# Kernel optimization log

Hardware: AMD Instinct MI355X
Metric: run time of the kernel (lower is better)

The kernel has to match this reference:

```python
import jax, jax.numpy as jnp
import numpy as np

B, C, H, W = 32, 64, 96, 96
RED = 8


def setup_inputs() -> dict:
    key = jax.random.key(0)
    k0, k1, k2 = jax.random.split(key, 3)
    x = jax.random.normal(k0, (B, C, H, W), dtype=jnp.float32)
    # 1x1 conv weights (squeezed to linear): conv1 C->C//RED, conv2 C//RED->C
    w1 = jax.random.normal(k1, (C // RED, C), dtype=jnp.float32) * (1.0 / np.sqrt(C))
    b1 = jnp.zeros((C // RED,), dtype=jnp.float32)
    w2 = jax.random.normal(k2, (C, C // RED), dtype=jnp.float32) * (1.0 / np.sqrt(C // RED))
    b2 = jnp.zeros((C,), dtype=jnp.float32)
    return {"x": x, "w1": w1, "b1": b1, "w2": w2, "b2": b2}


def reference(x, w1, b1, w2, b2):
    Bx, Cx, Hx, Wx = x.shape
    M = Hx * Wx
    # --- covariance pooling: x @ I_hat @ x^T == centered outer product / M ---
    xr = x.reshape(Bx, Cx, M)
    xc = xr - xr.mean(axis=-1, keepdims=True)
    cov = jnp.einsum('bcm,bdm->bcd', xc, xc) / M  # (B, C, C)
    # --- Newton-Schulz matrix sqrt, iteration = 5 ---
    I3 = 3.0 * jnp.eye(Cx, dtype=x.dtype)  # broadcast over batch
    normA = jnp.trace(cov, axis1=1, axis2=2)  # (1/3 * cov * 3I).sum == trace
    A = cov / normA[:, None, None]
    ZY = 0.5 * (I3 - A)
    Y = A @ ZY
    Z = ZY
    for _ in range(3):  # range(1, iteration-1) with iteration=5
        ZY = (0.5 * (I3 - Z)) @ Y
        Y = Y @ ZY
        Z = ZY @ Z
    ZY = 0.5 * (Y @ (I3 - Z @ Y))
    cov_sqrt = ZY * jnp.sqrt(normA)[:, None, None]  # (B, C, C)
    # --- channel gating ---
    s = cov_sqrt.mean(axis=1)  # mean over dim=1 -> (B, C)
    h = jax.nn.relu(s @ w1.T + b1)
    gate = jax.nn.sigmoid(h @ w2.T + b2)  # (B, C)
    return x * gate[:, :, None, None]
```

## Files before the change

kernel.cpp:

```cpp
#include <hip/hip_runtime.h>
#include <math.h>


#define BB 32
#define CC 64
#define MM 9216

typedef __attribute__((ext_vector_type(8))) short bf16x8;
typedef __attribute__((ext_vector_type(4))) float f32x4;

__device__ __forceinline__ short f2bf(float f) {
  unsigned u = __builtin_bit_cast(unsigned, f);
  return (short)(unsigned short)((u + 0x8000u) >> 16);
}
__device__ __forceinline__ float bf2f(short h) {
  unsigned u = ((unsigned)(unsigned short)h) << 16;
  return __builtin_bit_cast(float, u);
}

#define NCHUNK 8
#define CHUNK_M (MM / NCHUNK)
#define WAVE_M (CHUNK_M / 4)
#define NSTEP (WAVE_M / 32)

__global__ __launch_bounds__(256) void gram_k(const float* __restrict__ x,
                                              float* __restrict__ covws,
                                              float* __restrict__ sumws) {
  int b = blockIdx.x / NCHUNK;
  int chunk = blockIdx.x % NCHUNK;
  int tid = threadIdx.x;
  int w = tid >> 6, lane = tid & 63;
  int quad = lane >> 4, col = lane & 15;
  const float* xb = x + (size_t)b * CC * MM;
  int mwave = chunk * CHUNK_M + w * WAVE_M;

  f32x4 acc[4][4];
#pragma unroll
  for (int i = 0; i < 4; i++)
#pragma unroll
    for (int j = 0; j < 4; j++) acc[i][j] = (f32x4){0.f, 0.f, 0.f, 0.f};
  float csum[4] = {0.f, 0.f, 0.f, 0.f};

  const float* base[4];
#pragma unroll
  for (int rb = 0; rb < 4; rb++)
    base[rb] = xb + (size_t)(rb * 16 + col) * MM + mwave + quad * 8;

  float4 cur[4][2];
#pragma unroll
  for (int rb = 0; rb < 4; rb++) {
    cur[rb][0] = *(const float4*)(base[rb]);
    cur[rb][1] = *(const float4*)(base[rb] + 4);
  }
#pragma unroll
  for (int s = 0; s < NSTEP; s++) {
    float4 nxt[4][2];
    if (s + 1 < NSTEP) {
#pragma unroll
      for (int rb = 0; rb < 4; rb++) {
        const float* p = base[rb] + (s + 1) * 32;
        nxt[rb][0] = *(const float4*)(p);
        nxt[rb][1] = *(const float4*)(p + 4);
      }
    }
    bf16x8 frag[4];
#pragma unroll
    for (int rb = 0; rb < 4; rb++) {
      float v0 = cur[rb][0].x, v1 = cur[rb][0].y, v2 = cur[rb][0].z, v3 = cur[rb][0].w;
      float v4 = cur[rb][1].x, v5 = cur[rb][1].y, v6 = cur[rb][1].z, v7 = cur[rb][1].w;
      csum[rb] += ((v0 + v1) + (v2 + v3)) + ((v4 + v5) + (v6 + v7));
      bf16x8 f;
      f[0] = f2bf(v0); f[1] = f2bf(v1); f[2] = f2bf(v2); f[3] = f2bf(v3);
      f[4] = f2bf(v4); f[5] = f2bf(v5); f[6] = f2bf(v6); f[7] = f2bf(v7);
      frag[rb] = f;
    }
#pragma unroll
    for (int i = 0; i < 4; i++)
#pragma unroll
      for (int j = 0; j < 4; j++)
        acc[i][j] = __builtin_amdgcn_mfma_f32_16x16x32_bf16(frag[i], frag[j],
                                                            acc[i][j], 0, 0, 0);
    if (s + 1 < NSTEP) {
#pragma unroll
      for (int rb = 0; rb < 4; rb++) {
        cur[rb][0] = nxt[rb][0];
        cur[rb][1] = nxt[rb][1];
      }
    }
  }

  __shared__ float red[4][4096];
#pragma unroll
  for (int i = 0; i < 4; i++)
#pragma unroll
    for (int j = 0; j < 4; j++)
#pragma unroll
      for (int r = 0; r < 4; r++)
        red[w][(i * 16 + quad * 4 + r) * 64 + j * 16 + col] = acc[i][j][r];
  __syncthreads();
  float* covb = covws + b * 4096;
#pragma unroll
  for (int e = 0; e < 16; e++) {
    int idx = tid + 256 * e;
    float v = (red[0][idx] + red[1][idx]) + (red[2][idx] + red[3][idx]);
    atomicAdd(covb + idx, v);
  }
#pragma unroll
  for (int rb = 0; rb < 4; rb++) {
    float c0 = csum[rb];
    c0 += __shfl_xor(c0, 16);
    c0 += __shfl_xor(c0, 32);
    if (quad == 0 && w >= 0) {
      if (lane < 16) atomicAdd(sumws + b * 64 + rb * 16 + lane, c0);
    }
  }
}

__device__ __forceinline__ void mm64(short* __restrict__ D, const short* __restrict__ A,
                                     const short* __restrict__ Bm, int tid) {
  int w = tid >> 6, lane = tid & 63, quad = lane >> 4, col = lane & 15;
  f32x4 acc[4];
#pragma unroll
  for (int j = 0; j < 4; j++) acc[j] = (f32x4){0.f, 0.f, 0.f, 0.f};
#pragma unroll
  for (int ks = 0; ks < 2; ks++) {
    int k0 = ks * 32 + quad * 8;
    bf16x8 fa = *(const bf16x8*)(A + (w * 16 + col) * 64 + k0);
#pragma unroll
    for (int j = 0; j < 4; j++) {
      bf16x8 fb = *(const bf16x8*)(Bm + (j * 16 + col) * 64 + k0);
      acc[j] = __builtin_amdgcn_mfma_f32_16x16x32_bf16(fa, fb, acc[j], 0, 0, 0);
    }
  }
#pragma unroll
  for (int j = 0; j < 4; j++)
#pragma unroll
    for (int r = 0; r < 4; r++)
      D[(w * 16 + quad * 4 + r) * 64 + j * 16 + col] = f2bf(acc[j][r]);
}

__device__ __forceinline__ void mmcolsum(const short* __restrict__ A,
                                         const short* __restrict__ Bm,
                                         float* scol, int tid) {
  int w = tid >> 6, lane = tid & 63, quad = lane >> 4, col = lane & 15;
  f32x4 acc[4];
#pragma unroll
  for (int j = 0; j < 4; j++) acc[j] = (f32x4){0.f, 0.f, 0.f, 0.f};
#pragma unroll
  for (int ks = 0; ks < 2; ks++) {
    int k0 = ks * 32 + quad * 8;
    bf16x8 fa = *(const bf16x8*)(A + (w * 16 + col) * 64 + k0);
#pragma unroll
    for (int j = 0; j < 4; j++) {
      bf16x8 fb = *(const bf16x8*)(Bm + (j * 16 + col) * 64 + k0);
      acc[j] = __builtin_amdgcn_mfma_f32_16x16x32_bf16(fa, fb, acc[j], 0, 0, 0);
    }
  }
#pragma unroll
  for (int j = 0; j < 4; j++) {
    float t = (acc[j][0] + acc[j][1]) + (acc[j][2] + acc[j][3]);
    atomicAdd(&scol[j * 16 + col], t);
  }
}

__global__ __launch_bounds__(256) void ns_k(const float* __restrict__ covws,
                                            const float* __restrict__ sumws,
                                            const float* __restrict__ w1,
                                            const float* __restrict__ pb1,
                                            const float* __restrict__ w2,
                                            const float* __restrict__ pb2,
                                            float* __restrict__ gatews) {
  __shared__ __align__(16) short nb0[4096], nb1[4096], nb2[4096], nb3[4096], nb4[4096];
  __shared__ float mu[64];
  __shared__ float scol[64];
  __shared__ float hbuf[8];
  __shared__ float normA_sh;
  int b = blockIdx.x;
  int tid = threadIdx.x;
  const float* gram = covws + b * 4096;

  if (tid < 64) mu[tid] = sumws[b * 64 + tid] * (1.0f / MM);
  __syncthreads();
  if (tid < 64) {
    float d = gram[tid * 65] * (1.0f / MM) - mu[tid] * mu[tid];
#pragma unroll
    for (int off = 32; off >= 1; off >>= 1) d += __shfl_down(d, off);
    if (tid == 0) normA_sh = d;
  }
  __syncthreads();
  float rn = 1.0f / normA_sh;
#pragma unroll
  for (int e = 0; e < 16; e++) {
    int idx = tid + 256 * e;
    int r = idx >> 6, c = idx & 63;
    float cv = gram[idx] * (1.0f / MM) - mu[r] * mu[c];
    float a = cv * rn;
    nb0[idx] = f2bf(a);
    nb1[idx] = f2bf((r == c ? 1.5f : 0.0f) - 0.5f * a);
  }
  __syncthreads();
  mm64(nb2, nb0, nb1, tid);
  __syncthreads();
  short *pY = nb2, *pZ = nb1, *s0 = nb3, *s1 = nb4, *s2 = nb0;
  for (int it = 0; it < 3; ++it) {
#pragma unroll
    for (int e = 0; e < 16; e++) {
      int idx = tid + 256 * e;
      int r = idx >> 6, c = idx & 63;
      float z = bf2f(pZ[idx]);
      s0[idx] = f2bf((r == c ? 1.5f : 0.0f) - 0.5f * z);
    }
    __syncthreads();
    mm64(s1, s0, pY, tid);
    __syncthreads();
    mm64(s2, pY, s1, tid);
    mm64(s0, s1, pZ, tid);
    __syncthreads();
    short* oY = pY; short* oZ = pZ; short* oW = s1;
    pY = s2; pZ = s0; s0 = oY; s1 = oZ; s2 = oW;
  }
  mm64(s0, pZ, pY, tid);
  __syncthreads();
#pragma unroll
  for (int e = 0; e < 16; e++) {
    int idx = tid + 256 * e;
    int r = idx >> 6, c = idx & 63;
    float p = bf2f(s0[idx]);
    s0[idx] = f2bf((r == c ? 3.0f : 0.0f) - p);
  }
  if (tid < 64) scol[tid] = 0.0f;
  __syncthreads();
  mmcolsum(pY, s0, scol, tid);
  __syncthreads();
  if (tid < 8) {
    float sc = 0.5f * sqrtf(normA_sh) * (1.0f / 64.0f);
    float acc = pb1[tid];
    for (int c = 0; c < 64; c++) acc += scol[c] * sc * w1[tid * 64 + c];
    hbuf[tid] = fmaxf(acc, 0.0f);
  }
  __syncthreads();
  if (tid < 64) {
    float acc = pb2[tid];
#pragma unroll
    for (int j = 0; j < 8; j++) acc += hbuf[j] * w2[tid * 8 + j];
    gatews[b * 64 + tid] = 1.0f / (1.0f + __expf(-acc));
  }
}

#define N4 (BB * CC * MM / 4)
__global__ __launch_bounds__(256) void gate_mul(const float* __restrict__ x,
                                                const float* __restrict__ gatews,
                                                float* __restrict__ out) {
  int i = blockIdx.x * 256 + threadIdx.x;
  int bc = i / 2304;
  float g = gatews[bc];
  float4 v = ((const float4*)x)[i];
  v.x *= g; v.y *= g; v.z *= g; v.w *= g;
  ((float4*)out)[i] = v;
}

extern "C" void kernel_launch(void* const* d_in, const int* in_sizes, int n_in,
                              void* d_out, int out_size, void* d_ws, size_t ws_size,
                              hipStream_t stream) {
  const float* x = (const float*)d_in[0];
  const float* w1 = (const float*)d_in[1];
  const float* b1 = (const float*)d_in[2];
  const float* w2 = (const float*)d_in[3];
  const float* b2 = (const float*)d_in[4];
  float* out = (float*)d_out;
  float* ws = (float*)d_ws;
  float* covws = ws;
  float* sumws = ws + BB * 4096;
  float* gatews = sumws + BB * 64;

  hipMemsetAsync(ws, 0, (size_t)(BB * 4096 + BB * 64) * sizeof(float), stream);
  gram_k<<<BB * NCHUNK, 256, 0, stream>>>(x, covws, sumws);
  ns_k<<<BB, 256, 0, stream>>>(covws, sumws, w1, b1, w2, b2, gatews);
  gate_mul<<<N4 / 256, 256, 0, stream>>>(x, gatews, out);
}
```

Baseline: 164.5 us.

## Split Gram reduction into more chunks with per-chunk partials instead of atomics

Raises the number of M-chunks per batch from 8 to 24 so more blocks fill the GPU, and sets a launch bound of 3 blocks per SM. Each block now writes its partial Gram matrix and channel sums to its own workspace slot instead of issuing global atomicAdds, and the NS kernel sums the 24 partials. This also removes the memset and halves the shared reduction buffer by having two waves accumulate into the other two waves' slots. The bf16 conversion is replaced by packing pairs with truncation rather than rounding. The costs are a larger workspace, extra partial-sum reads in ns_k, and slightly lower precision.

```diff
diff --git a/kernel.cpp b/kernel.cpp
--- a/kernel.cpp
+++ b/kernel.cpp
@@ -17,15 +17,20 @@
   unsigned u = ((unsigned)(unsigned short)h) << 16;
   return __builtin_bit_cast(float, u);
 }
-
-#define NCHUNK 8
+__device__ __forceinline__ unsigned pack2(float lo, float hi) {
+  unsigned ul = __builtin_bit_cast(unsigned, lo);
+  unsigned uh = __builtin_bit_cast(unsigned, hi);
+  return (uh & 0xffff0000u) | (ul >> 16);
+}
+
+#define NCHUNK 24
 #define CHUNK_M (MM / NCHUNK)
 #define WAVE_M (CHUNK_M / 4)
 #define NSTEP (WAVE_M / 32)
 
-__global__ __launch_bounds__(256) void gram_k(const float* __restrict__ x,
-                                              float* __restrict__ covws,
-                                              float* __restrict__ sumws) {
+__global__ __launch_bounds__(256, 3) void gram_k(const float* __restrict__ x,
+                                                 float* __restrict__ covpart,
+                                                 float* __restrict__ sumpart) {
   int b = blockIdx.x / NCHUNK;
   int chunk = blockIdx.x % NCHUNK;
   int tid = threadIdx.x;
@@ -70,8 +75,11 @@
       float v4 = cur[rb][1].x, v5 = cur[rb][1].y, v6 = cur[rb][1].z, v7 = cur[rb][1].w;
       csum[rb] += ((v0 + v1) + (v2 + v3)) + ((v4 + v5) + (v6 + v7));
       bf16x8 f;
-      f[0] = f2bf(v0); f[1] = f2bf(v1); f[2] = f2bf(v2); f[3] = f2bf(v3);
-      f[4] = f2bf(v4); f[5] = f2bf(v5); f[6] = f2bf(v6); f[7] = f2bf(v7);
+      unsigned* fu = (unsigned*)&f;
+      fu[0] = pack2(v0, v1);
+      fu[1] = pack2(v2, v3);
+      fu[2] = pack2(v4, v5);
+      fu[3] = pack2(v6, v7);
       frag[rb] = f;
     }
 #pragma unroll
@@ -89,31 +97,48 @@
     }
   }
 
-  __shared__ float red[4][4096];
-#pragma unroll
-  for (int i = 0; i < 4; i++)
-#pragma unroll
-    for (int j = 0; j < 4; j++)
-#pragma unroll
-      for (int r = 0; r < 4; r++)
-        red[w][(i * 16 + quad * 4 + r) * 64 + j * 16 + col] = acc[i][j][r];
-  __syncthreads();
-  float* covb = covws + b * 4096;
-#pragma unroll
-  for (int e = 0; e < 16; e++) {
-    int idx = tid + 256 * e;
-    float v = (red[0][idx] + red[1][idx]) + (red[2][idx] + red[3][idx]);
-    atomicAdd(covb + idx, v);
+  __shared__ float red[2][4096];
+  __shared__ float swave[4][64];
+  if (w >= 2) {
+#pragma unroll
+    for (int i = 0; i < 4; i++)
+#pragma unroll
+      for (int j = 0; j < 4; j++)
+#pragma unroll
+        for (int r = 0; r < 4; r++)
+          red[w - 2][(i * 16 + quad * 4 + r) * 64 + j * 16 + col] = acc[i][j][r];
   }
 #pragma unroll
   for (int rb = 0; rb < 4; rb++) {
     float c0 = csum[rb];
     c0 += __shfl_xor(c0, 16);
     c0 += __shfl_xor(c0, 32);
-    if (quad == 0 && w >= 0) {
-      if (lane < 16) atomicAdd(sumws + b * 64 + rb * 16 + lane, c0);
-    }
-  }
+    if (lane < 16) swave[w][rb * 16 + lane] = c0;
+  }
+  __syncthreads();
+  if (w < 2) {
+#pragma unroll
+    for (int i = 0; i < 4; i++)
+#pragma unroll
+      for (int j = 0; j < 4; j++)
+#pragma unroll
+        for (int r = 0; r < 4; r++)
+          red[w][(i * 16 + quad * 4 + r) * 64 + j * 16 + col] += acc[i][j][r];
+  }
+  __syncthreads();
+  float4* cp = (float4*)(covpart + (size_t)(b * NCHUNK + chunk) * 4096);
+  const float4* r0 = (const float4*)red[0];
+  const float4* r1 = (const float4*)red[1];
+#pragma unroll
+  for (int e = 0; e < 4; e++) {
+    int idx = tid + 256 * e;
+    float4 a = r0[idx], bb = r1[idx];
+    a.x += bb.x; a.y += bb.y; a.z += bb.z; a.w += bb.w;
+    cp[idx] = a;
+  }
+  if (tid < 64)
+    sumpart[(size_t)(b * NCHUNK + chunk) * 64 + tid] =
+        ((swave[0][tid] + swave[1][tid]) + (swave[2][tid] + swave[3][tid]));
 }
 
 __device__ __forceinline__ void mm64(short* __restrict__ D, const short* __restrict__ A,
@@ -163,26 +188,42 @@
   }
 }
 
-__global__ __launch_bounds__(256) void ns_k(const float* __restrict__ covws,
-                                            const float* __restrict__ sumws,
+__global__ __launch_bounds__(256) void ns_k(const float* __restrict__ covpart,
+                                            const float* __restrict__ sumpart,
                                             const float* __restrict__ w1,
                                             const float* __restrict__ pb1,
                                             const float* __restrict__ w2,
                                             const float* __restrict__ pb2,
                                             float* __restrict__ gatews) {
   __shared__ __align__(16) short nb0[4096], nb1[4096], nb2[4096], nb3[4096], nb4[4096];
+  __shared__ __align__(16) float gbuf[4096];
   __shared__ float mu[64];
   __shared__ float scol[64];
   __shared__ float hbuf[8];
   __shared__ float normA_sh;
   int b = blockIdx.x;
   int tid = threadIdx.x;
-  const float* gram = covws + b * 4096;
-
-  if (tid < 64) mu[tid] = sumws[b * 64 + tid] * (1.0f / MM);
-  __syncthreads();
+
+  const float4* cp = (const float4*)covpart + (size_t)b * NCHUNK * 1024;
+  float4* gb4 = (float4*)gbuf;
+#pragma unroll
+  for (int e = 0; e < 4; e++) {
+    int idx = tid + 256 * e;
+    float4 s = {0.f, 0.f, 0.f, 0.f};
+    for (int ch = 0; ch < NCHUNK; ch++) {
+      float4 v = cp[(size_t)ch * 1024 + idx];
+      s.x += v.x; s.y += v.y; s.z += v.z; s.w += v.w;
+    }
+    gb4[idx] = s;
+  }
   if (tid < 64) {
-    float d = gram[tid * 65] * (1.0f / MM) - mu[tid] * mu[tid];
+    float s = 0.f;
+    for (int ch = 0; ch < NCHUNK; ch++) s += sumpart[(size_t)(b * NCHUNK + ch) * 64 + tid];
+    mu[tid] = s * (1.0f / MM);
+  }
+  __syncthreads();
+  if (tid < 64) {
+    float d = gbuf[tid * 65] * (1.0f / MM) - mu[tid] * mu[tid];
 #pragma unroll
     for (int off = 32; off >= 1; off >>= 1) d += __shfl_down(d, off);
     if (tid == 0) normA_sh = d;
@@ -193,7 +234,7 @@
   for (int e = 0; e < 16; e++) {
     int idx = tid + 256 * e;
     int r = idx >> 6, c = idx & 63;
-    float cv = gram[idx] * (1.0f / MM) - mu[r] * mu[c];
+    float cv = gbuf[idx] * (1.0f / MM) - mu[r] * mu[c];
     float a = cv * rn;
     nb0[idx] = f2bf(a);
     nb1[idx] = f2bf((r == c ? 1.5f : 0.0f) - 0.5f * a);
@@ -269,12 +310,11 @@
   const float* b2 = (const float*)d_in[4];
   float* out = (float*)d_out;
   float* ws = (float*)d_ws;
-  float* covws = ws;
-  float* sumws = ws + BB * 4096;
-  float* gatews = sumws + BB * 64;
-
-  hipMemsetAsync(ws, 0, (size_t)(BB * 4096 + BB * 64) * sizeof(float), stream);
-  gram_k<<<BB * NCHUNK, 256, 0, stream>>>(x, covws, sumws);
-  ns_k<<<BB, 256, 0, stream>>>(covws, sumws, w1, b1, w2, b2, gatews);
+  float* covpart = ws;
+  float* sumpart = covpart + (size_t)BB * NCHUNK * 4096;
+  float* gatews = sumpart + (size_t)BB * NCHUNK * 64;
+
+  gram_k<<<BB * NCHUNK, 256, 0, stream>>>(x, covpart, sumpart);
+  ns_k<<<BB, 256, 0, stream>>>(covpart, sumpart, w1, b1, w2, b2, gatews);
   gate_mul<<<N4 / 256, 256, 0, stream>>>(x, gatews, out);
 }
```

After: 192.5 us. 17.0% more time.
